# Performance work log

Hardware: AMD Instinct MI355X
Metric: run time of the kernel (lower is better)

## Reference

```python
import jax, jax.numpy as jnp
import numpy as np

MIN_NORM = 1e-15
EPS = 1e-7  # artanh domain clamp for fp32


def _tan_k(u, k):
    sk = jnp.sqrt(-k)
    return jnp.tanh(jnp.clip(sk * u, -15.0, 15.0)) / sk


def _artan_k(u, k):
    sk = jnp.sqrt(-k)
    return jnp.arctanh(jnp.clip(sk * u, -1.0 + EPS, 1.0 - EPS)) / sk


def _norm(x):
    return jnp.maximum(jnp.linalg.norm(x, axis=-1, keepdims=True), MIN_NORM)


def mobius_add(x, y, k):
    x2 = jnp.sum(x * x, axis=-1, keepdims=True)
    y2 = jnp.sum(y * y, axis=-1, keepdims=True)
    xy = jnp.sum(x * y, axis=-1, keepdims=True)
    num = (1.0 - 2.0 * k * xy - k * y2) * x + (1.0 + k * x2) * y
    den = 1.0 - 2.0 * k * xy + k * k * x2 * y2
    return num / jnp.maximum(den, MIN_NORM)


def mobius_matvec(M, x, k):
    # x: [..., d_in], M: [d_out, d_in]
    xn = _norm(x)
    mx = x @ M.T
    mxn = _norm(mx)
    res = _tan_k(mxn / xn * _artan_k(xn, k), k) * (mx / mxn)
    return jnp.where(jnp.all(mx == 0.0, axis=-1, keepdims=True), 0.0, res)


def mobius_pointwise_mul(w, x, k):
    xn = _norm(x)
    wx = w * x
    wxn = _norm(wx)
    res = _tan_k(wxn / xn * _artan_k(xn, k), k) * (wx / wxn)
    return jnp.where(jnp.all(wx == 0.0, axis=-1, keepdims=True), 0.0, res)


def expmap0(u, k):
    un = _norm(u)
    return _tan_k(un, k) * u / un


def logmap0(y, k):
    yn = _norm(y)
    return _artan_k(yn, k) * y / yn


def one_rnn_transform(W, h, U, x, b, k):
    Wh = mobius_matvec(W, h, k)
    Ux = mobius_matvec(U, x, k)
    return mobius_add(mobius_add(Wh, Ux, k), b, k)


def mobius_gru_cell(x, hx, w_ih, w_hh, b, k):
    W_ir, W_ih_, W_iz = jnp.split(w_ih, 3, axis=0)
    W_hr, W_hh_, W_hz = jnp.split(w_hh, 3, axis=0)
    b_r, b_h, b_z = b[0], b[1], b[2]
    z_t = jax.nn.sigmoid(logmap0(one_rnn_transform(W_hz, hx, W_iz, x, b_z, k), k))
    r_t = jax.nn.sigmoid(logmap0(one_rnn_transform(W_hr, hx, W_ir, x, b_r, k), k))
    rh_t = mobius_pointwise_mul(r_t, hx, k)
    h_tilde = one_rnn_transform(W_hh_, rh_t, W_ih_, x, b_h, k)
    delta_h = mobius_add(-hx, h_tilde, k)
    return mobius_add(hx, mobius_pointwise_mul(z_t, delta_h, k), k)


def mobius_gru_layer(x_tbd, h0, w_ih, w_hh, b, k, hyperbolic_input):
    # x_tbd: [T, B, D]; h0: [B, H]
    if not hyperbolic_input:
        x_tbd = expmap0(x_tbd, k)

    def step(hx, xt):
        h = expmap0(hx, k)
        h = mobius_gru_cell(xt, h, w_ih, w_hh, b, k)
        h = logmap0(h, k)
        return h, h

    h_last, outs = jax.lax.scan(step, h0, x_tbd)
    return outs, h_last  # outs: [T, B, H]


def setup_inputs() -> dict:
    key = jax.random.key(0)
    ks = jax.random.split(key, 8)
    B, T, D, H = 64, 1024, 256, 256
    stdv = 1.0 / np.sqrt(H)
    x = 0.02 * jax.random.normal(ks[0], (B, T, D), dtype=jnp.float32)
    k = jnp.float32(-1.0)  # hyperbolic curvature (geoopt sign convention)
    h0 = jnp.zeros((2, B, H), dtype=jnp.float32)
    w_ih0 = jax.random.uniform(ks[1], (3 * H, D), jnp.float32, -stdv, stdv)
    w_hh0 = jax.random.uniform(ks[2], (3 * H, H), jnp.float32, -stdv, stdv)
    b0 = 1e-5 * jax.random.normal(ks[3], (3, H), dtype=jnp.float32)
    w_ih1 = jax.random.uniform(ks[4], (3 * H, H), jnp.float32, -stdv, stdv)
    w_hh1 = jax.random.uniform(ks[5], (3 * H, H), jnp.float32, -stdv, stdv)
    b1 = 1e-5 * jax.random.normal(ks[6], (3, H), dtype=jnp.float32)
    return {"x": x, "k": k, "h0": h0, "w_ih0": w_ih0, "w_hh0": w_hh0, "b0": b0,
            "w_ih1": w_ih1, "w_hh1": w_hh1, "b1": b1}


def reference(x, k, h0, w_ih0, w_hh0, b0, w_ih1, w_hh1, b1):
    # x: [B, T, D]; source unbinds dim 1 as time -> scan over time-major.
    xt = jnp.swapaxes(x, 0, 1)  # [T, B, D]
    out0, hl0 = mobius_gru_layer(xt, h0[0], w_ih0, w_hh0, b0, k, hyperbolic_input=False)
    out1, hl1 = mobius_gru_layer(out0, h0[1], w_ih1, w_hh1, b1, k, hyperbolic_input=True)
    ht = jnp.stack([hl0, hl1])  # [num_layers, B, H]
    return out1, ht
```

## Files before the change

### kernel.cpp

```cpp
#include <hip/hip_runtime.h>
#include <cstdint>
#include <cstddef>

#define MINN 1e-15f
#define EPSA 1e-7f
#define C_L2E 1.44269504088896341f
#define C_LN2 0.69314718055994531f

typedef _Float16 half_t;
typedef _Float16 half2_t __attribute__((ext_vector_type(2)));

#if defined(__has_builtin)
#if __has_builtin(__builtin_amdgcn_update_dpp) && __has_builtin(__builtin_amdgcn_readlane)
#define USE_DPP 1
#endif
#endif

__device__ __forceinline__ float fexp2_(float x) {
#if defined(__has_builtin) && __has_builtin(__builtin_amdgcn_exp2f)
    return __builtin_amdgcn_exp2f(x);
#else
    return exp2f(x);
#endif
}
__device__ __forceinline__ float flog2_(float x) {
#if defined(__has_builtin) && __has_builtin(__builtin_amdgcn_logf)
    return __builtin_amdgcn_logf(x);
#else
    return log2f(x);
#endif
}
__device__ __forceinline__ float frcp_(float x) {
#if defined(__has_builtin) && __has_builtin(__builtin_amdgcn_rcpf)
    return __builtin_amdgcn_rcpf(x);
#else
    return 1.f / x;
#endif
}
__device__ __forceinline__ float tan_k_(float u, float sk, float rsk) {
    float a = fminf(fmaxf(sk * u, -15.f), 15.f);
    float t = fexp2_(a * (2.f * C_L2E));
    return (1.f - 2.f * frcp_(t + 1.f)) * rsk;
}
__device__ __forceinline__ float artan_k_(float u, float sk, float rsk) {
    float a = fminf(fmaxf(sk * u, -1.f + EPSA), 1.f - EPSA);
    return flog2_((1.f + a) * frcp_(1.f - a)) * (0.5f * C_LN2) * rsk;
}
__device__ __forceinline__ float sigm_(float x) {
    return frcp_(1.f + fexp2_(-x * C_L2E));
}
__device__ __forceinline__ float wave_sum(float v) {
#pragma unroll
    for (int off = 32; off; off >>= 1) v += __shfl_xor(v, off, 64);
    return v;
}

#ifdef USE_DPP
template <int CTRL, int RM, int BM>
__device__ __forceinline__ float dppmov_(float x) {
    return __builtin_bit_cast(float,
        __builtin_amdgcn_update_dpp(0, __builtin_bit_cast(int, x), CTRL, RM, BM, false));
}
#endif
__device__ __forceinline__ float wsum63_(float x) {
#ifdef USE_DPP
    x += dppmov_<0x111, 0xf, 0xf>(x);
    x += dppmov_<0x112, 0xf, 0xf>(x);
    x += dppmov_<0x114, 0xf, 0xe>(x);
    x += dppmov_<0x118, 0xf, 0xc>(x);
    x += dppmov_<0x142, 0xa, 0xf>(x);
    x += dppmov_<0x143, 0xc, 0xf>(x);
    return x;
#else
    return wave_sum(x);
#endif
}
__device__ __forceinline__ float gsum8_(float x) {
#ifdef USE_DPP
    x += dppmov_<0x111, 0xf, 0xf>(x);
    x += dppmov_<0x112, 0xf, 0xf>(x);
    x += dppmov_<0x114, 0xf, 0xe>(x);
    return x;
#else
    x += __shfl_xor(x, 1, 64);
    x += __shfl_xor(x, 2, 64);
    x += __shfl_xor(x, 4, 64);
    return x;
#endif
}
__device__ __forceinline__ float rdlane_(float x, int l) {
#ifdef USE_DPP
    return __builtin_bit_cast(float,
        __builtin_amdgcn_readlane(__builtin_bit_cast(int, x), l));
#else
    return __shfl(x, l, 64);
#endif
}
template <int N>
__device__ __forceinline__ void bredX(float* v, float* redbuf, int tid) {
    const int lane = tid & 63, wave = tid >> 6;
#pragma unroll
    for (int n = 0; n < N; ++n) {
        float s = wsum63_(v[n]);
        if (lane == 63) redbuf[n * 8 + wave] = s;
    }
    __syncthreads();
    float part = redbuf[lane & (8 * N - 1)];
    part = gsum8_(part);
#pragma unroll
    for (int n = 0; n < N; ++n) v[n] = rdlane_(part, 8 * n + 7);
}

__device__ __forceinline__ float dot2acc(uint32_t w, uint32_t h, float acc) {
#if defined(__has_builtin) && __has_builtin(__builtin_amdgcn_fdot2)
    return __builtin_amdgcn_fdot2(__builtin_bit_cast(half2_t, w),
                                  __builtin_bit_cast(half2_t, h), acc, false);
#else
    half2_t a = __builtin_bit_cast(half2_t, w);
    half2_t b = __builtin_bit_cast(half2_t, h);
    acc = fmaf((float)a[0], (float)b[0], acc);
    return fmaf((float)a[1], (float)b[1], acc);
#endif
}

__global__ __launch_bounds__(256) void kt_transpose(
    const float* __restrict__ a0, const float* __restrict__ a1,
    float* __restrict__ o0, float* __restrict__ o1) {
    int idx = blockIdx.x * 256 + threadIdx.x;
    int m = idx / 196608, rem = idx % 196608;
    int j = rem >> 8, kk = rem & 255;
    const float* in = (m == 0) ? a0 : a1;
    float* outp     = (m == 0) ? o0 : o1;
    outp[kk * 768 + j] = in[j * 256 + kk];
}

__global__ __launch_bounds__(256) void kt_prep1(
    const float* __restrict__ whh0, const float* __restrict__ whh1,
    uint32_t* __restrict__ p0, uint32_t* __restrict__ p1) {
    int idx = blockIdx.x * 256 + threadIdx.x;
    int l = idx >> 16, e = idx & 65535;
    int r4 = e >> 11, rem = e & 2047;
    int t = rem >> 2, m = r4 * 4 + (rem & 3);
    int lane = t & 63, wave = t >> 6;
    int p = wave * 32 + (lane & 31), ph = lane >> 5;
    int g = m >> 6, mi = m & 63;
    int row = g ? (512 + p) : p;
    int i = ph * 128 + 2 * mi;
    const float* w = l ? whh1 : whh0;
    half2_t hv;
    hv[0] = (half_t)w[row * 256 + i];
    hv[1] = (half_t)w[row * 256 + i + 1];
    (l ? p1 : p0)[e] = __builtin_bit_cast(uint32_t, hv);
}

__global__ __launch_bounds__(256) void kt_prep2(
    const float* __restrict__ whh0, const float* __restrict__ whh1,
    uint32_t* __restrict__ p0, uint32_t* __restrict__ p1) {
    int idx = blockIdx.x * 256 + threadIdx.x;
    int l = idx >> 15, e = idx & 32767;
    int i2 = e >> 8, j = e & 255;
    const float* w = l ? whh1 : whh0;
    half2_t hv;
    hv[0] = (half_t)w[(256 + j) * 256 + 2 * i2];
    hv[1] = (half_t)w[(256 + j) * 256 + 2 * i2 + 1];
    (l ? p1 : p0)[e] = __builtin_bit_cast(uint32_t, hv);
}

__global__ __launch_bounds__(256) void kt_init(
    const float* __restrict__ h0, float* __restrict__ hcar) {
    int i = blockIdx.x * 256 + threadIdx.x;
    hcar[i] = h0[i];
}
__global__ __launch_bounds__(256) void kt_final(
    const float* __restrict__ hcar, float* __restrict__ dst) {
    int i = blockIdx.x * 256 + threadIdx.x;
    dst[i] = hcar[i];
}

__global__ __launch_bounds__(256) void kt_rowscale(
    const float* __restrict__ src, long long strideB,
    float* __restrict__ s_arr, float* __restrict__ ax_arr,
    const float* __restrict__ kptr, int mode) {
    int lane = threadIdx.x & 63;
    int r = blockIdx.x * 4 + (threadIdx.x >> 6);
    float k = kptr[0], sk = sqrtf(-k), rsk = frcp_(sk);
    size_t off = (size_t)(r >> 6) * strideB + (size_t)(r & 63) * 256 + lane * 4;
    float4 v = *(const float4*)&src[off];
    float n2 = wave_sum(v.x * v.x + v.y * v.y + v.z * v.z + v.w * v.w);
    float n = sqrtf(n2);
    float s, xn;
    if (mode == 0) {
        float nrm = fmaxf(n, MINN);
        float tk = tan_k_(nrm, sk, rsk);
        s = tk * frcp_(nrm);
        xn = fmaxf(tk * (n * frcp_(nrm)), MINN);
    } else {
        s = 1.f;
        xn = fmaxf(n, MINN);
    }
    float ax = artan_k_(xn, sk, rsk) * frcp_(xn);
    if (lane == 0) { s_arr[r] = s; ax_arr[r] = ax; }
}

__global__ __launch_bounds__(256) void kt_gemm(
    const float* __restrict__ A, long long strideB,
    const float* __restrict__ s_arr,
    const float* __restrict__ Bt, float* __restrict__ C) {
    __shared__ float As[16][68];
    __shared__ float Bs[16][68];
    __shared__ float sS[64];
    int tid = threadIdx.x;
    int row0 = blockIdx.y * 64, col0 = blockIdx.x * 64;
    if (tid < 64) sS[tid] = s_arr[row0 + tid];
    int ty = tid >> 4, tx = tid & 15;
    int ra = tid >> 2, kq = tid & 3;
    int kb = tid >> 4, cq = tid & 15;
    float acc[4][4] = {};
    __syncthreads();
#pragma unroll 1
    for (int kt = 0; kt < 16; ++kt) {
        int k0 = kt * 16;
        int rc = row0 + ra;
        size_t aoff = (size_t)(rc >> 6) * strideB + (size_t)(rc & 63) * 256 + k0 + kq * 4;
        float4 av = *(const float4*)&A[aoff];
        float sc = sS[ra];
        float4 bv = *(const float4*)&Bt[(size_t)(k0 + kb) * 768 + col0 + cq * 4];
        As[kq * 4 + 0][ra] = av.x * sc;
        As[kq * 4 + 1][ra] = av.y * sc;
        As[kq * 4 + 2][ra] = av.z * sc;
        As[kq * 4 + 3][ra] = av.w * sc;
        *(float4*)&Bs[kb][cq * 4] = bv;
        __syncthreads();
#pragma unroll
        for (int kk = 0; kk < 16; ++kk) {
            float4 a4 = *(const float4*)&As[kk][ty * 4];
            float4 b4 = *(const float4*)&Bs[kk][tx * 4];
            float aa[4] = {a4.x, a4.y, a4.z, a4.w};
            float bb[4] = {b4.x, b4.y, b4.z, b4.w};
#pragma unroll
            for (int i = 0; i < 4; ++i)
#pragma unroll
                for (int j = 0; j < 4; ++j)
                    acc[i][j] = fmaf(aa[i], bb[j], acc[i][j]);
        }
        __syncthreads();
    }
#pragma unroll
    for (int i = 0; i < 4; ++i) {
        size_t row = (size_t)row0 + ty * 4 + i;
        *(float4*)&C[row * 768 + col0 + tx * 4] =
            make_float4(acc[i][0], acc[i][1], acc[i][2], acc[i][3]);
    }
}

__global__ __launch_bounds__(256) void kt_mscale(
    float* __restrict__ mx, const float* __restrict__ ax_arr,
    float* __restrict__ uxn, float* __restrict__ uxb,
    const float* __restrict__ bias, const float* __restrict__ kptr) {
    int lane = threadIdx.x & 63;
    int p = blockIdx.x * 4 + (threadIdx.x >> 6);
    int r = p / 3;
    int g = p - r * 3;
    float k = kptr[0], sk = sqrtf(-k), rsk = frcp_(sk);
    float* ptr = mx + (size_t)r * 768 + g * 256 + lane * 4;
    float4 v = *(const float4*)ptr;
    float4 b4 = *(const float4*)&bias[g * 256 + lane * 4];
    float n2 = wave_sum(v.x * v.x + v.y * v.y + v.z * v.z + v.w * v.w);
    float vb = wave_sum(v.x * b4.x + v.y * b4.y + v.z * b4.z + v.w * b4.w);
    float nt = sqrtf(n2);
    float mxn = fmaxf(nt, MINN);
    float arg = mxn * ax_arr[r];
    float tk = tan_k_(arg, sk, rsk);
    float f = tk * frcp_(mxn);
    v.x *= f; v.y *= f; v.z *= f; v.w *= f;
    *(float4*)ptr = v;
    if (lane == 0) { uxn[p] = tk * (nt * frcp_(mxn)); uxb[p] = f * vb; }
}

__global__ __launch_bounds__(512, 1) void kt_scan2(
    const float* __restrict__ Ux_0, const float* __restrict__ uxn_0,
    const float* __restrict__ uxb_0,
    const uint32_t* __restrict__ w1pk_0, const uint32_t* __restrict__ whh2g_0,
    const float* __restrict__ bias_0, float* __restrict__ hcar_0,
    float* __restrict__ out_0, long long sb_0, long long st_0,
    const float* __restrict__ Ux_1, const float* __restrict__ uxn_1,
    const float* __restrict__ uxb_1,
    const uint32_t* __restrict__ w1pk_1, const uint32_t* __restrict__ whh2g_1,
    const float* __restrict__ bias_1, float* __restrict__ hcar_1,
    float* __restrict__ out_1, long long sb_1, long long st_1,
    const float* __restrict__ kptr, int Tc, int nrole0) {
    __shared__ uint4 whhS[8192];
    __shared__ uint32_t hy2S[128];
    __shared__ uint32_t rh2S[128];
    __shared__ float redbuf[2][64];

    const int tid = threadIdx.x;
    const int role = (blockIdx.x >= nrole0) ? 1 : 0;
    const int bb = role ? (int)blockIdx.x - nrole0 : (int)blockIdx.x;

    const float* Ux      = role ? Ux_1 : Ux_0;
    const float* uxn     = role ? uxn_1 : uxn_0;
    const float* uxb     = role ? uxb_1 : uxb_0;
    const uint32_t* w1pk = role ? w1pk_1 : w1pk_0;
    const uint32_t* whh2g= role ? whh2g_1 : whh2g_0;
    const float* bias    = role ? bias_1 : bias_0;
    float* hcar          = role ? hcar_1 : hcar_0;
    float* outbase       = role ? out_1 : out_0;
    const long long stride_b = role ? sb_1 : sb_0;
    const long long stride_t = role ? st_1 : st_0;

    const int lane = tid & 63, wave = tid >> 6;
    const int p = wave * 32 + (lane & 31), ph = lane >> 5;
    const float k = kptr[0], sk = sqrtf(-k), rsk = frcp_(sk);

    for (int idx = tid; idx < 32768; idx += 512) {
        uint32_t v = whh2g[idx];
        int i2 = idx >> 8, col = idx & 255;
        ((uint32_t*)whhS)[((i2 >> 2) * 256 + col) * 4 + (i2 & 3)] = v;
    }
    uint32_t w1[128];
    {
        const uint4* wp = (const uint4*)w1pk;
#pragma unroll
        for (int r4 = 0; r4 < 32; ++r4) {
            uint4 v = wp[r4 * 512 + tid];
            w1[4 * r4 + 0] = v.x; w1[4 * r4 + 1] = v.y;
            w1[4 * r4 + 2] = v.z; w1[4 * r4 + 3] = v.w;
        }
    }

    const float br = bias[p], bh = bias[256 + p], bz = bias[512 + p];
    float h = hcar[bb * 256 + p];
    __syncthreads();
    float v4[4] = {br * br, bh * bh, bz * bz, h * h};
    bredX<4>(v4, redbuf[0], tid);
    const float bn2r = 0.5f * v4[0], bn2h = 0.5f * v4[1], bn2z = 0.5f * v4[2];
    float S_h2 = 0.5f * v4[3];

    float* myout = outbase + (size_t)bb * stride_b;
    const float* uxpb = Ux + (size_t)bb * Tc * 768;
    const float* unpb = uxn + (size_t)bb * Tc * 3;
    const float* ubpb = uxb + (size_t)bb * Tc * 3;

    float puxr = uxpb[p], puxh = uxpb[256 + p], puxz = uxpb[512 + p];
    float punr = unpb[0], punh = unpb[1], punz = unpb[2];
    float pubr = ubpb[0], pubh = ubpb[1], pubz = ubpb[2];

    for (int t = 0; t < Tc; ++t) {
        const float uxr = puxr, uxh = puxh, uxz = puxz;
        const float unr = punr, unh = punh, unz = punz;
        const float S_ubr = pubr, S_ubh = pubh, S_ubz = pubz;

        float hn = sqrtf(S_h2);
        float nrm = fmaxf(hn, MINN);
        float tk0 = tan_k_(nrm, sk, rsk);
        float chy = tk0 * frcp_(nrm);
        float hy = chy * h;
        float Shy2 = chy * chy * S_h2;
        float xnh = fmaxf(tk0 * (hn * frcp_(nrm)), MINN);
        float axh = artan_k_(xnh, sk, rsk) * frcp_(xnh);
        if (ph == 0) ((half_t*)hy2S)[p] = (half_t)hy;
        __syncthreads();

        if (t + 1 < Tc) {
            const float* uxp2 = uxpb + (size_t)(t + 1) * 768;
            puxr = uxp2[p]; puxh = uxp2[256 + p]; puxz = uxp2[512 + p];
            const float* unp2 = unpb + (size_t)(t + 1) * 3;
            punr = unp2[0]; punh = unp2[1]; punz = unp2[2];
            const float* ubp2 = ubpb + (size_t)(t + 1) * 3;
            pubr = ubp2[0]; pubh = ubp2[1]; pubz = ubp2[2];
        }

        float pr0 = 0.f, pr1 = 0.f, pz0 = 0.f, pz1 = 0.f;
        {
            const uint4* hp = (const uint4*)hy2S + ph * 16;
#pragma unroll
            for (int c4 = 0; c4 < 4; ++c4) {
                uint32_t hv[16];
#pragma unroll
                for (int u = 0; u < 4; ++u) {
                    uint4 v = hp[c4 * 4 + u];
                    hv[4 * u + 0] = v.x; hv[4 * u + 1] = v.y;
                    hv[4 * u + 2] = v.z; hv[4 * u + 3] = v.w;
                }
#pragma unroll
                for (int m = 0; m < 16; ++m) {
                    if (c4 < 2) {
                        pr0 = dot2acc(w1[c4 * 16 + m], hv[m], pr0);
                        pz0 = dot2acc(w1[64 + c4 * 16 + m], hv[m], pz0);
                    } else {
                        pr1 = dot2acc(w1[c4 * 16 + m], hv[m], pr1);
                        pz1 = dot2acc(w1[64 + c4 * 16 + m], hv[m], pz1);
                    }
                }
            }
        }
        float pr = pr0 + pr1, pz = pz0 + pz1;
        const float mr = pr + __shfl_xor(pr, 32, 64);
        const float mz = pz + __shfl_xor(pz, 32, 64);

        float vr[8] = {mr * mr, mz * mz, mr * uxr, mz * uxz,
                       mr * br, mz * bz, h * uxh, h * bh};
        bredX<8>(vr, redbuf[0], tid);
        const float S_mr2 = 0.5f * vr[0], S_mz2 = 0.5f * vr[1];
        const float S_mru = 0.5f * vr[2], S_mzu = 0.5f * vr[3];
        const float S_mrb = 0.5f * vr[4], S_mzb = 0.5f * vr[5];
        const float S_huxh = 0.5f * vr[6], S_hbh = 0.5f * vr[7];

        float r_t, z_t;
        {
            float mxn = fmaxf(sqrtf(S_mr2), MINN);
            float tk = tan_k_(mxn * axh, sk, rsk);
            float f = tk * frcp_(mxn);
            float x2 = f * f * S_mr2, y2 = unr * unr, xy = f * S_mru;
            float a = 1.f - 2.f * k * xy - k * y2;
            float bq = 1.f + k * x2;
            float rd = frcp_(fmaxf(1.f - 2.f * k * xy + k * k * x2 * y2, MINN));
            float c1 = (a * f * mr + bq * uxr) * rd;
            float Sc12 = (a * a * x2 + 2.f * a * bq * xy + bq * bq * y2) * (rd * rd);
            float Sc1b = (a * f * S_mrb + bq * S_ubr) * rd;
            float g = 1.f - 2.f * k * Sc1b - k * bn2r;
            float dl = 1.f + k * Sc12;
            float re = frcp_(fmaxf(1.f - 2.f * k * Sc1b + k * k * Sc12 * bn2r, MINN));
            float c2 = (g * c1 + dl * br) * re;
            float Sc22 = (g * g * Sc12 + 2.f * g * dl * Sc1b + dl * dl * bn2r) * (re * re);
            float yn = fmaxf(sqrtf(Sc22), MINN);
            float lr = artan_k_(yn, sk, rsk) * frcp_(yn) * c2;
            r_t = sigm_(lr);
        }
        {
            float mxn = fmaxf(sqrtf(S_mz2), MINN);
            float tk = tan_k_(mxn * axh, sk, rsk);
            float f = tk * frcp_(mxn);
            float x2 = f * f * S_mz2, y2 = unz * unz, xy = f * S_mzu;
            float a = 1.f - 2.f * k * xy - k * y2;
            float bq = 1.f + k * x2;
            float rd = frcp_(fmaxf(1.f - 2.f * k * xy + k * k * x2 * y2, MINN));
            float c1 = (a * f * mz + bq * uxz) * rd;
            float Sc12 = (a * a * x2 + 2.f * a * bq * xy + bq * bq * y2) * (rd * rd);
            float Sc1b = (a * f * S_mzb + bq * S_ubz) * rd;
            float g = 1.f - 2.f * k * Sc1b - k * bn2z;
            float dl = 1.f + k * Sc12;
            float re = frcp_(fmaxf(1.f - 2.f * k * Sc1b + k * k * Sc12 * bn2z, MINN));
            float c2 = (g * c1 + dl * bz) * re;
            float Sc22 = (g * g * Sc12 + 2.f * g * dl * Sc1b + dl * dl * bn2z) * (re * re);
            float yn = fmaxf(sqrtf(Sc22), MINN);
            float lz = artan_k_(yn, sk, rsk) * frcp_(yn) * c2;
            z_t = sigm_(lz);
        }

        float wx = r_t * hy;
        if (ph == 0) ((half_t*)rh2S)[p] = (half_t)wx;
        {
            float s1v = wsum63_(wx * wx);
            if (lane == 63) redbuf[1][wave] = s1v;
        }
        __syncthreads();

        float part1 = gsum8_(redbuf[1][lane & 7]);
        const float S_wx2 = 0.5f * rdlane_(part1, 7);
        float wxt = sqrtf(S_wx2);
        float wxn = fmaxf(wxt, MINN);
        float tkw = tan_k_(wxn * axh, sk, rsk);
        float fw = tkw * frcp_(wxn);
        float rhn = tkw * (wxt * frcp_(wxn));

        float q0 = 0.f, q1 = 0.f;
        {
            const uint4* rp = (const uint4*)rh2S + ph * 16;
#pragma unroll
            for (int u = 0; u < 16; ++u) {
                uint4 wv = whhS[(ph * 16 + u) * 256 + p];
                uint4 rv = rp[u];
                if (u < 8) {
                    q0 = dot2acc(wv.x, rv.x, q0);
                    q0 = dot2acc(wv.y, rv.y, q0);
                    q0 = dot2acc(wv.z, rv.z, q0);
                    q0 = dot2acc(wv.w, rv.w, q0);
                } else {
                    q1 = dot2acc(wv.x, rv.x, q1);
                    q1 = dot2acc(wv.y, rv.y, q1);
                    q1 = dot2acc(wv.z, rv.z, q1);
                    q1 = dot2acc(wv.w, rv.w, q1);
                }
            }
        }
        float qq = q0 + q1;
        const float mh = fw * (qq + __shfl_xor(qq, 32, 64));

        float v4b[4] = {mh * mh, mh * uxh, mh * bh, hy * mh};
        bredX<4>(v4b, redbuf[0], tid);
        const float S_mh2 = 0.5f * v4b[0], S_mhu = 0.5f * v4b[1];
        const float S_mhb = 0.5f * v4b[2], S_hymh = 0.5f * v4b[3];

        float wz, Sdelta2;
        {
            float xnrh = fmaxf(rhn, MINN);
            float axrh = artan_k_(xnrh, sk, rsk) * frcp_(xnrh);
            float mxn = fmaxf(sqrtf(S_mh2), MINN);
            float tk = tan_k_(mxn * axrh, sk, rsk);
            float f = tk * frcp_(mxn);
            float x2 = f * f * S_mh2, y2 = unh * unh, xy = f * S_mhu;
            float a = 1.f - 2.f * k * xy - k * y2;
            float bq = 1.f + k * x2;
            float rd = frcp_(fmaxf(1.f - 2.f * k * xy + k * k * x2 * y2, MINN));
            float c1 = (a * f * mh + bq * uxh) * rd;
            float Sc12 = (a * a * x2 + 2.f * a * bq * xy + bq * bq * y2) * (rd * rd);
            float Sc1b = (a * f * S_mhb + bq * S_ubh) * rd;
            float S_hyc1 = (a * f * S_hymh + bq * chy * S_huxh) * rd;
            float g = 1.f - 2.f * k * Sc1b - k * bn2h;
            float dl = 1.f + k * Sc12;
            float re = frcp_(fmaxf(1.f - 2.f * k * Sc1b + k * k * Sc12 * bn2h, MINN));
            float htl = (g * c1 + dl * bh) * re;
            float Shtl2 = (g * g * Sc12 + 2.f * g * dl * Sc1b + dl * dl * bn2h) * (re * re);
            float S_hyhtl = (g * S_hyc1 + dl * chy * S_hbh) * re;
            float ad = 1.f + 2.f * k * S_hyhtl - k * Shtl2;
            float bd = 1.f + k * Shy2;
            float rdd = frcp_(fmaxf(1.f + 2.f * k * S_hyhtl + k * k * Shy2 * Shtl2, MINN));
            float delta = (ad * (-hy) + bd * htl) * rdd;
            Sdelta2 = (ad * ad * Shy2 - 2.f * ad * bd * S_hyhtl + bd * bd * Shtl2) * (rdd * rdd);
            wz = z_t * delta;
        }
        float v2[2] = {wz * wz, hy * wz};
        bredX<2>(v2, redbuf[1], tid);
        const float S_wz2 = 0.5f * v2[0], S_hywz = 0.5f * v2[1];

        {
            float dnc = fmaxf(sqrtf(Sdelta2), MINN);
            float axd = artan_k_(dnc, sk, rsk) * frcp_(dnc);
            float wzt = sqrtf(S_wz2);
            float wznc = fmaxf(wzt, MINN);
            float tkzd = tan_k_(wznc * axd, sk, rsk);
            float fz = tkzd * frcp_(wznc);
            float zd = fz * wz;
            float zdn2 = fz * fz * S_wz2;
            float S_hyzd = fz * S_hywz;
            float an = 1.f - 2.f * k * S_hyzd - k * zdn2;
            float bn_ = 1.f + k * Shy2;
            float rdn = frcp_(fmaxf(1.f - 2.f * k * S_hyzd + k * k * Shy2 * zdn2, MINN));
            float hnew = (an * hy + bn_ * zd) * rdn;
            float Shnew2 = (an * an * Shy2 + 2.f * an * bn_ * S_hyzd + bn_ * bn_ * zdn2) * (rdn * rdn);
            float yn = fmaxf(sqrtf(Shnew2), MINN);
            float ayn = artan_k_(yn, sk, rsk) * frcp_(yn);
            float outv = ayn * hnew;
            if (ph == 0) myout[(size_t)t * stride_t + p] = outv;
            h = outv;
            S_h2 = ayn * ayn * Shnew2;
        }
    }
    if (ph == 0) hcar[bb * 256 + p] = h;
}

extern "C" void kernel_launch(void* const* d_in, const int* in_sizes, int n_in,
                              void* d_out, int out_size, void* d_ws, size_t ws_size,
                              hipStream_t stream) {
    const float* x    = (const float*)d_in[0];
    const float* kptr = (const float*)d_in[1];
    const float* h0   = (const float*)d_in[2];
    const float* wih0 = (const float*)d_in[3];
    const float* whh0 = (const float*)d_in[4];
    const float* b0   = (const float*)d_in[5];
    const float* wih1 = (const float*)d_in[6];
    const float* whh1 = (const float*)d_in[7];
    const float* b1   = (const float*)d_in[8];
    float* out = (float*)d_out;
    float* ws  = (float*)d_ws;

    const int B = 64, T = 1024, H = 256;
    const int CT = 64, NC = 16;
    const int RC = B * CT;

    float* wt_ih0 = ws;
    float* wt_ih1 = wt_ih0 + 196608;
    uint32_t* w1pk0  = (uint32_t*)(wt_ih1 + 196608);
    uint32_t* w1pk1  = w1pk0 + 65536;
    uint32_t* whh2g0 = w1pk1 + 65536;
    uint32_t* whh2g1 = whh2g0 + 32768;
    float* hcar  = (float*)(whh2g1 + 32768);
    float* s0    = hcar + 32768;
    float* ax0   = s0 + RC;
    float* s1    = ax0 + RC;
    float* ax1   = s1 + RC;
    float* uxn0  = ax1 + RC;
    float* uxn1  = uxn0 + 3 * RC;
    float* uxb0  = uxn1 + 3 * RC;
    float* uxb1  = uxb0 + 3 * RC;
    float* out0c = uxb1 + 3 * RC;
    float* mx0   = out0c + (size_t)RC * H;
    float* mx1   = mx0 + (size_t)RC * 768;

    float* hcar0 = hcar;
    float* hcar1 = hcar + (size_t)B * H;

    dim3 blk(256);
    kt_transpose<<<dim3(1536), blk, 0, stream>>>(wih0, wih1, wt_ih0, wt_ih1);
    kt_prep1<<<dim3(512), blk, 0, stream>>>(whh0, whh1, w1pk0, w1pk1);
    kt_prep2<<<dim3(256), blk, 0, stream>>>(whh0, whh1, whh2g0, whh2g1);
    kt_init<<<dim3(128), blk, 0, stream>>>(h0, hcar);

    const long long sbx = (long long)T * 256;
    const long long sbc = (long long)CT * 256;

    {
        const float* xc = x;
        kt_rowscale<<<dim3(RC / 4), blk, 0, stream>>>(xc, sbx, s0, ax0, kptr, 0);
        kt_gemm<<<dim3(12, RC / 64), blk, 0, stream>>>(xc, sbx, s0, wt_ih0, mx0);
        kt_mscale<<<dim3(RC * 3 / 4), blk, 0, stream>>>(mx0, ax0, uxn0, uxb0, b0, kptr);
        kt_scan2<<<dim3(B), dim3(512), 0, stream>>>(
            mx0, uxn0, uxb0, w1pk0, whh2g0, b0, hcar0, out0c, sbc, 256LL,
            mx0, uxn0, uxb0, w1pk0, whh2g0, b0, hcar0, out0c, sbc, 256LL,
            kptr, CT, B);
    }
    for (int c = 1; c < NC; ++c) {
        const float* xc = x + (size_t)c * CT * 256;
        kt_rowscale<<<dim3(RC / 4), blk, 0, stream>>>(xc, sbx, s0, ax0, kptr, 0);
        kt_gemm<<<dim3(12, RC / 64), blk, 0, stream>>>(xc, sbx, s0, wt_ih0, mx0);
        kt_mscale<<<dim3(RC * 3 / 4), blk, 0, stream>>>(mx0, ax0, uxn0, uxb0, b0, kptr);
        kt_rowscale<<<dim3(RC / 4), blk, 0, stream>>>(out0c, sbc, s1, ax1, kptr, 1);
        kt_gemm<<<dim3(12, RC / 64), blk, 0, stream>>>(out0c, sbc, s1, wt_ih1, mx1);
        kt_mscale<<<dim3(RC * 3 / 4), blk, 0, stream>>>(mx1, ax1, uxn1, uxb1, b1, kptr);
        kt_scan2<<<dim3(2 * B), dim3(512), 0, stream>>>(
            mx0, uxn0, uxb0, w1pk0, whh2g0, b0, hcar0, out0c, sbc, 256LL,
            mx1, uxn1, uxb1, w1pk1, whh2g1, b1, hcar1,
            out + (size_t)(c - 1) * CT * B * H, 256LL, (long long)B * H,
            kptr, CT, B);
    }
    {
        kt_rowscale<<<dim3(RC / 4), blk, 0, stream>>>(out0c, sbc, s1, ax1, kptr, 1);
        kt_gemm<<<dim3(12, RC / 64), blk, 0, stream>>>(out0c, sbc, s1, wt_ih1, mx1);
        kt_mscale<<<dim3(RC * 3 / 4), blk, 0, stream>>>(mx1, ax1, uxn1, uxb1, b1, kptr);
        kt_scan2<<<dim3(B), dim3(512), 0, stream>>>(
            mx1, uxn1, uxb1, w1pk1, whh2g1, b1, hcar1,
            out + (size_t)(NC - 1) * CT * B * H, 256LL, (long long)B * H,
            mx1, uxn1, uxb1, w1pk1, whh2g1, b1, hcar1,
            out + (size_t)(NC - 1) * CT * B * H, 256LL, (long long)B * H,
            kptr, CT, B);
    }
    kt_final<<<dim3(128), blk, 0, stream>>>(hcar, out + (size_t)T * B * H);
}
```

Baseline: 6.298 ms.

## Fuse row-norm scaling into GEMM and split GRU gate math across half-waves

Removes the separate kt_rowscale kernel: each GEMM block now computes the row norms, scale factors and artanh terms for its own 64 rows before the tile loop. Every column block recomputes these and writes ax redundantly, but 32 launches go away. In the scan kernel, the two halves of the block each evaluate one gate (r or z) and swap results with a cross-lane shuffle, instead of every thread evaluating both. The dot-product accumulators are also split into four independent chains to shorten dependency latency.

```diff
diff --git a/kernel.cpp b/kernel.cpp
--- a/kernel.cpp
+++ b/kernel.cpp
@@ -177,41 +177,44 @@
     dst[i] = hcar[i];
 }
 
-__global__ __launch_bounds__(256) void kt_rowscale(
-    const float* __restrict__ src, long long strideB,
-    float* __restrict__ s_arr, float* __restrict__ ax_arr,
-    const float* __restrict__ kptr, int mode) {
-    int lane = threadIdx.x & 63;
-    int r = blockIdx.x * 4 + (threadIdx.x >> 6);
-    float k = kptr[0], sk = sqrtf(-k), rsk = frcp_(sk);
-    size_t off = (size_t)(r >> 6) * strideB + (size_t)(r & 63) * 256 + lane * 4;
-    float4 v = *(const float4*)&src[off];
-    float n2 = wave_sum(v.x * v.x + v.y * v.y + v.z * v.z + v.w * v.w);
-    float n = sqrtf(n2);
-    float s, xn;
-    if (mode == 0) {
-        float nrm = fmaxf(n, MINN);
-        float tk = tan_k_(nrm, sk, rsk);
-        s = tk * frcp_(nrm);
-        xn = fmaxf(tk * (n * frcp_(nrm)), MINN);
-    } else {
-        s = 1.f;
-        xn = fmaxf(n, MINN);
-    }
-    float ax = artan_k_(xn, sk, rsk) * frcp_(xn);
-    if (lane == 0) { s_arr[r] = s; ax_arr[r] = ax; }
-}
-
 __global__ __launch_bounds__(256) void kt_gemm(
     const float* __restrict__ A, long long strideB,
-    const float* __restrict__ s_arr,
-    const float* __restrict__ Bt, float* __restrict__ C) {
+    const float* __restrict__ Bt, float* __restrict__ C,
+    float* __restrict__ ax_arr, const float* __restrict__ kptr, int mode) {
     __shared__ float As[16][68];
     __shared__ float Bs[16][68];
     __shared__ float sS[64];
     int tid = threadIdx.x;
     int row0 = blockIdx.y * 64, col0 = blockIdx.x * 64;
-    if (tid < 64) sS[tid] = s_arr[row0 + tid];
+
+    {
+        float kk = kptr[0], sk = sqrtf(-kk), rsk = frcp_(sk);
+        int row = tid >> 2, q = tid & 3;
+        int rc = row0 + row;
+        size_t base = (size_t)(rc >> 6) * strideB + (size_t)(rc & 63) * 256 + q * 64;
+        float n2 = 0.f;
+#pragma unroll
+        for (int u = 0; u < 16; ++u) {
+            float4 v = *(const float4*)&A[base + u * 4];
+            n2 += v.x * v.x + v.y * v.y + v.z * v.z + v.w * v.w;
+        }
+        n2 += __shfl_xor(n2, 1, 64);
+        n2 += __shfl_xor(n2, 2, 64);
+        float n = sqrtf(n2);
+        float s, xn;
+        if (mode == 0) {
+            float nrm = fmaxf(n, MINN);
+            float tk = tan_k_(nrm, sk, rsk);
+            s = tk * frcp_(nrm);
+            xn = fmaxf(tk * (n * frcp_(nrm)), MINN);
+        } else {
+            s = 1.f;
+            xn = fmaxf(n, MINN);
+        }
+        float ax = artan_k_(xn, sk, rsk) * frcp_(xn);
+        if (q == 0) { sS[row] = s; ax_arr[rc] = ax; }
+    }
+
     int ty = tid >> 4, tx = tid & 15;
     int ra = tid >> 2, kq = tid & 3;
     int kb = tid >> 4, cq = tid & 15;
@@ -371,7 +374,8 @@
             pubr = ubp2[0]; pubh = ubp2[1]; pubz = ubp2[2];
         }
 
-        float pr0 = 0.f, pr1 = 0.f, pz0 = 0.f, pz1 = 0.f;
+        float prA[4] = {0.f, 0.f, 0.f, 0.f};
+        float pzA[4] = {0.f, 0.f, 0.f, 0.f};
         {
             const uint4* hp = (const uint4*)hy2S + ph * 16;
 #pragma unroll
@@ -385,17 +389,13 @@
                 }
 #pragma unroll
                 for (int m = 0; m < 16; ++m) {
-                    if (c4 < 2) {
-                        pr0 = dot2acc(w1[c4 * 16 + m], hv[m], pr0);
-                        pz0 = dot2acc(w1[64 + c4 * 16 + m], hv[m], pz0);
-                    } else {
-                        pr1 = dot2acc(w1[c4 * 16 + m], hv[m], pr1);
-                        pz1 = dot2acc(w1[64 + c4 * 16 + m], hv[m], pz1);
-                    }
+                    prA[c4] = dot2acc(w1[c4 * 16 + m], hv[m], prA[c4]);
+                    pzA[c4] = dot2acc(w1[64 + c4 * 16 + m], hv[m], pzA[c4]);
                 }
             }
         }
-        float pr = pr0 + pr1, pz = pz0 + pz1;
+        float pr = (prA[0] + prA[1]) + (prA[2] + prA[3]);
+        float pz = (pzA[0] + pzA[1]) + (pzA[2] + pzA[3]);
         const float mr = pr + __shfl_xor(pr, 32, 64);
         const float mz = pz + __shfl_xor(pz, 32, 64);
 
@@ -407,47 +407,39 @@
         const float S_mrb = 0.5f * vr[4], S_mzb = 0.5f * vr[5];
         const float S_huxh = 0.5f * vr[6], S_hbh = 0.5f * vr[7];
 
-        float r_t, z_t;
+        const float m_   = ph ? mz    : mr;
+        const float S2_  = ph ? S_mz2 : S_mr2;
+        const float Su_  = ph ? S_mzu : S_mru;
+        const float Sb_  = ph ? S_mzb : S_mrb;
+        const float Sub_ = ph ? S_ubz : S_ubr;
+        const float bn2_ = ph ? bn2z  : bn2r;
+        const float un_  = ph ? unz   : unr;
+        const float ux_  = ph ? uxz   : uxr;
+        const float b_   = ph ? bz    : br;
+        float g_own;
         {
-            float mxn = fmaxf(sqrtf(S_mr2), MINN);
+            float mxn = fmaxf(sqrtf(S2_), MINN);
             float tk = tan_k_(mxn * axh, sk, rsk);
             float f = tk * frcp_(mxn);
-            float x2 = f * f * S_mr2, y2 = unr * unr, xy = f * S_mru;
+            float x2 = f * f * S2_, y2 = un_ * un_, xy = f * Su_;
             float a = 1.f - 2.f * k * xy - k * y2;
             float bq = 1.f + k * x2;
             float rd = frcp_(fmaxf(1.f - 2.f * k * xy + k * k * x2 * y2, MINN));
-            float c1 = (a * f * mr + bq * uxr) * rd;
+            float c1 = (a * f * m_ + bq * ux_) * rd;
             float Sc12 = (a * a * x2 + 2.f * a * bq * xy + bq * bq * y2) * (rd * rd);
-            float Sc1b = (a * f * S_mrb + bq * S_ubr) * rd;
-            float g = 1.f - 2.f * k * Sc1b - k * bn2r;
+            float Sc1b = (a * f * Sb_ + bq * Sub_) * rd;
+            float g = 1.f - 2.f * k * Sc1b - k * bn2_;
             float dl = 1.f + k * Sc12;
-            float re = frcp_(fmaxf(1.f - 2.f * k * Sc1b + k * k * Sc12 * bn2r, MINN));
-            float c2 = (g * c1 + dl * br) * re;
-            float Sc22 = (g * g * Sc12 + 2.f * g * dl * Sc1b + dl * dl * bn2r) * (re * re);
+            float re = frcp_(fmaxf(1.f - 2.f * k * Sc1b + k * k * Sc12 * bn2_, MINN));
+            float c2 = (g * c1 + dl * b_) * re;
+            float Sc22 = (g * g * Sc12 + 2.f * g * dl * Sc1b + dl * dl * bn2_) * (re * re);
             float yn = fmaxf(sqrtf(Sc22), MINN);
-            float lr = artan_k_(yn, sk, rsk) * frcp_(yn) * c2;
-            r_t = sigm_(lr);
-        }
-        {
-            float mxn = fmaxf(sqrtf(S_mz2), MINN);
-            float tk = tan_k_(mxn * axh, sk, rsk);
-            float f = tk * frcp_(mxn);
-            float x2 = f * f * S_mz2, y2 = unz * unz, xy = f * S_mzu;
-            float a = 1.f - 2.f * k * xy - k * y2;
-            float bq = 1.f + k * x2;
-            float rd = frcp_(fmaxf(1.f - 2.f * k * xy + k * k * x2 * y2, MINN));
-            float c1 = (a * f * mz + bq * uxz) * rd;
-            float Sc12 = (a * a * x2 + 2.f * a * bq * xy + bq * bq * y2) * (rd * rd);
-            float Sc1b = (a * f * S_mzb + bq * S_ubz) * rd;
-            float g = 1.f - 2.f * k * Sc1b - k * bn2z;
-            float dl = 1.f + k * Sc12;
-            float re = frcp_(fmaxf(1.f - 2.f * k * Sc1b + k * k * Sc12 * bn2z, MINN));
-            float c2 = (g * c1 + dl * bz) * re;
-            float Sc22 = (g * g * Sc12 + 2.f * g * dl * Sc1b + dl * dl * bn2z) * (re * re);
-            float yn = fmaxf(sqrtf(Sc22), MINN);
-            float lz = artan_k_(yn, sk, rsk) * frcp_(yn) * c2;
-            z_t = sigm_(lz);
-        }
+            float lg = artan_k_(yn, sk, rsk) * frcp_(yn) * c2;
+            g_own = sigm_(lg);
+        }
+        const float g_oth = __shfl_xor(g_own, 32, 64);
+        const float r_t = ph ? g_oth : g_own;
+        const float z_t = ph ? g_own : g_oth;
 
         float wx = r_t * hy;
         if (ph == 0) ((half_t*)rh2S)[p] = (half_t)wx;
@@ -465,27 +457,21 @@
         float fw = tkw * frcp_(wxn);
         float rhn = tkw * (wxt * frcp_(wxn));
 
-        float q0 = 0.f, q1 = 0.f;
+        float qA[4] = {0.f, 0.f, 0.f, 0.f};
         {
             const uint4* rp = (const uint4*)rh2S + ph * 16;
 #pragma unroll
             for (int u = 0; u < 16; ++u) {
                 uint4 wv = whhS[(ph * 16 + u) * 256 + p];
                 uint4 rv = rp[u];
-                if (u < 8) {
-                    q0 = dot2acc(wv.x, rv.x, q0);
-                    q0 = dot2acc(wv.y, rv.y, q0);
-                    q0 = dot2acc(wv.z, rv.z, q0);
-                    q0 = dot2acc(wv.w, rv.w, q0);
-                } else {
-                    q1 = dot2acc(wv.x, rv.x, q1);
-                    q1 = dot2acc(wv.y, rv.y, q1);
-                    q1 = dot2acc(wv.z, rv.z, q1);
-                    q1 = dot2acc(wv.w, rv.w, q1);
-                }
+                int s = u >> 2;
+                qA[s] = dot2acc(wv.x, rv.x, qA[s]);
+                qA[s] = dot2acc(wv.y, rv.y, qA[s]);
+                qA[s] = dot2acc(wv.z, rv.z, qA[s]);
+                qA[s] = dot2acc(wv.w, rv.w, qA[s]);
             }
         }
-        float qq = q0 + q1;
+        float qq = (qA[0] + qA[1]) + (qA[2] + qA[3]);
         const float mh = fw * (qq + __shfl_xor(qq, 32, 64));
 
         float v4b[4] = {mh * mh, mh * uxh, mh * bh, hy * mh};
@@ -577,10 +563,8 @@
     uint32_t* whh2g0 = w1pk1 + 65536;
     uint32_t* whh2g1 = whh2g0 + 32768;
     float* hcar  = (float*)(whh2g1 + 32768);
-    float* s0    = hcar + 32768;
-    float* ax0   = s0 + RC;
-    float* s1    = ax0 + RC;
-    float* ax1   = s1 + RC;
+    float* ax0   = hcar + 32768;
+    float* ax1   = ax0 + RC;
     float* uxn0  = ax1 + RC;
     float* uxn1  = uxn0 + 3 * RC;
     float* uxb0  = uxn1 + 3 * RC;
@@ -603,8 +587,7 @@
 
     {
         const float* xc = x;
-        kt_rowscale<<<dim3(RC / 4), blk, 0, stream>>>(xc, sbx, s0, ax0, kptr, 0);
-        kt_gemm<<<dim3(12, RC / 64), blk, 0, stream>>>(xc, sbx, s0, wt_ih0, mx0);
+        kt_gemm<<<dim3(12, RC / 64), blk, 0, stream>>>(xc, sbx, wt_ih0, mx0, ax0, kptr, 0);
         kt_mscale<<<dim3(RC * 3 / 4), blk, 0, stream>>>(mx0, ax0, uxn0, uxb0, b0, kptr);
         kt_scan2<<<dim3(B), dim3(512), 0, stream>>>(
             mx0, uxn0, uxb0, w1pk0, whh2g0, b0, hcar0, out0c, sbc, 256LL,
@@ -613,11 +596,9 @@
     }
     for (int c = 1; c < NC; ++c) {
         const float* xc = x + (size_t)c * CT * 256;
-        kt_rowscale<<<dim3(RC / 4), blk, 0, stream>>>(xc, sbx, s0, ax0, kptr, 0);
-        kt_gemm<<<dim3(12, RC / 64), blk, 0, stream>>>(xc, sbx, s0, wt_ih0, mx0);
+        kt_gemm<<<dim3(12, RC / 64), blk, 0, stream>>>(xc, sbx, wt_ih0, mx0, ax0, kptr, 0);
         kt_mscale<<<dim3(RC * 3 / 4), blk, 0, stream>>>(mx0, ax0, uxn0, uxb0, b0, kptr);
-        kt_rowscale<<<dim3(RC / 4), blk, 0, stream>>>(out0c, sbc, s1, ax1, kptr, 1);
-        kt_gemm<<<dim3(12, RC / 64), blk, 0, stream>>>(out0c, sbc, s1, wt_ih1, mx1);
+        kt_gemm<<<dim3(12, RC / 64), blk, 0, stream>>>(out0c, sbc, wt_ih1, mx1, ax1, kptr, 1);
         kt_mscale<<<dim3(RC * 3 / 4), blk, 0, stream>>>(mx1, ax1, uxn1, uxb1, b1, kptr);
         kt_scan2<<<dim3(2 * B), dim3(512), 0, stream>>>(
             mx0, uxn0, uxb0, w1pk0, whh2g0, b0, hcar0, out0c, sbc, 256LL,
@@ -626,8 +607,7 @@
             kptr, CT, B);
     }
     {
-        kt_rowscale<<<dim3(RC / 4), blk, 0, stream>>>(out0c, sbc, s1, ax1, kptr, 1);
-        kt_gemm<<<dim3(12, RC / 64), blk, 0, stream>>>(out0c, sbc, s1, wt_ih1, mx1);
+        kt_gemm<<<dim3(12, RC / 64), blk, 0, stream>>>(out0c, sbc, wt_ih1, mx1, ax1, kptr, 1);
         kt_mscale<<<dim3(RC * 3 / 4), blk, 0, stream>>>(mx1, ax1, uxn1, uxb1, b1, kptr);
         kt_scan2<<<dim3(B), dim3(512), 0, stream>>>(
             mx1, uxn1, uxb1, w1pk1, whh2g1, b1, hcar1,
```

Result: faster. 6.134 ms (-2.6%).
